# Kernel tuning notes

Measured on AMD Instinct MI355X. Metric: run time of the kernel, lower is better.

The kernel has to match this reference:

```python
import jax, jax.numpy as jnp
import numpy as np

HIDDEN = 2048
HEADS = 16
HEAD_DIM = HIDDEN // HEADS  # 128
ROPE_BASE = 10000.0
RMS_EPS = 1e-6
MINUS_INF = -10000.0


def rms_norm(x, w):
    xf = x.astype(jnp.float32)
    var = jnp.mean(xf * xf, axis=-1, keepdims=True)
    return w * (x * jax.lax.rsqrt(var + RMS_EPS))


def rotate_half(x):
    x1, x2 = jnp.split(x, 2, axis=-1)
    return jnp.concatenate((-x2, x1), axis=-1)


def rope_tables(seq_len, dtype):
    inv_freq = 1.0 / (ROPE_BASE ** (jnp.arange(0, HEAD_DIM, 2, dtype=jnp.float32) / HEAD_DIM))
    t = jnp.arange(seq_len, dtype=jnp.float32)
    freqs = jnp.einsum('i,j->ij', t, inv_freq)           # [S, D/2]
    emb = jnp.concatenate((freqs, freqs), axis=-1)       # [S, D]
    return jnp.cos(emb).astype(dtype), jnp.sin(emb).astype(dtype)


def setup_inputs() -> dict:
    key = jax.random.key(0)
    ks = jax.random.split(key, 6)
    B, S, H = 2, 2048, HIDDEN
    x = jax.random.normal(ks[0], (B, S, H), dtype=jnp.float32) * 0.5
    norm_w = jnp.ones((H,), dtype=jnp.float32)
    scale = 0.02
    wq = jax.random.normal(ks[1], (H, H), dtype=jnp.float32) * scale
    wk = jax.random.normal(ks[2], (H, H), dtype=jnp.float32) * scale
    wv = jax.random.normal(ks[3], (H, H), dtype=jnp.float32) * scale
    wo = jax.random.normal(ks[4], (H, H), dtype=jnp.float32) * scale
    position_ids = jnp.broadcast_to(jnp.arange(S, dtype=jnp.int32), (B, S))
    return {"x": x, "norm_w": norm_w, "wq": wq, "wk": wk, "wv": wv,
            "wo": wo, "position_ids": position_ids}


def reference(x, norm_w, wq, wk, wv, wo, position_ids):
    B, S, H = x.shape
    h = rms_norm(x, norm_w)
    # torch Linear: y = h @ W.T, weight is [out, in]
    def proj(w):
        return jnp.einsum('bsd,od->bso', h, w).reshape(B, S, HEADS, HEAD_DIM).transpose(0, 2, 1, 3)
    q, k, v = proj(wq), proj(wk), proj(wv)  # [B, Hh, S, D]
    cos, sin = rope_tables(S, x.dtype)
    cos = cos[position_ids][:, None]  # [B, 1, S, D]
    sin = sin[position_ids][:, None]
    q = q * cos + rotate_half(q) * sin
    k = k * cos + rotate_half(k) * sin
    scores = jnp.einsum('bhqd,bhkd->bhqk', q, k) / jnp.sqrt(jnp.float32(HEAD_DIM))
    causal = jnp.tril(jnp.ones((S, S), dtype=bool))
    scores = scores + jnp.where(causal, 0.0, MINUS_INF).astype(scores.dtype)
    probs = jax.nn.softmax(scores, axis=-1)
    ctx = jnp.einsum('bhqk,bhkd->bhqd', probs, v)          # [B, Hh, S, D]
    ctx = ctx.transpose(0, 2, 1, 3).reshape(B, S, H)
    out = jnp.einsum('bsd,od->bso', ctx, wo)
    return out
```

## Files before the change

kernel.cpp:

```cpp
#include <hip/hip_runtime.h>
#include <hip/hip_bf16.h>
#include <stdint.h>

#define S_LEN   2048
#define BATCH   2
#define HID     2048
#define NHEADS  16
#define HDIM    128
#define ROWS    (BATCH * S_LEN)
#define QS      6144
#define ATT_SCALE 0.08838834764831843f

typedef __attribute__((ext_vector_type(8))) short s16x8;
typedef __attribute__((ext_vector_type(4))) float f32x4;

#define GLL16(gp, lp)                                                          \
  __builtin_amdgcn_global_load_lds(                                            \
      (__attribute__((address_space(1))) void*)(gp),                           \
      (__attribute__((address_space(3))) void*)(lp), 16, 0, 0)

__device__ __forceinline__ float bf2f(unsigned short u) {
  union { unsigned int i; float f; } v; v.i = ((unsigned int)u) << 16; return v.f;
}
__device__ __forceinline__ unsigned short f2bf(float f) {
  union { float f; unsigned int i; } v; v.f = f;
  unsigned int i = v.i;
  return (unsigned short)((i + 0x7FFFu + ((i >> 16) & 1u)) >> 16);
}
__device__ __forceinline__ void store_out(unsigned short* p, float v) { *p = f2bf(v); }
__device__ __forceinline__ void store_out(float* p, float v) { *p = v; }

__global__ __launch_bounds__(256) void cast_w_kernel(const float* __restrict__ in,
                                                     unsigned short* __restrict__ out, int n4) {
  int i = blockIdx.x * 256 + threadIdx.x;
  if (i >= n4) return;
  float4 v = ((const float4*)in)[i];
  ushort4 o;
  o.x = f2bf(v.x); o.y = f2bf(v.y); o.z = f2bf(v.z); o.w = f2bf(v.w);
  ((ushort4*)out)[i] = o;
}

__global__ __launch_bounds__(256) void rmsnorm_kernel(const float* __restrict__ x,
                                                      const float* __restrict__ w,
                                                      unsigned short* __restrict__ h) {
  int row = blockIdx.x;
  int t = threadIdx.x;
  const float4* xr4 = (const float4*)(x + (size_t)row * HID);
  float4 a = xr4[t], b = xr4[t + 256];
  float ss = a.x*a.x + a.y*a.y + a.z*a.z + a.w*a.w
           + b.x*b.x + b.y*b.y + b.z*b.z + b.w*b.w;
#pragma unroll
  for (int off = 32; off >= 1; off >>= 1) ss += __shfl_xor(ss, off, 64);
  __shared__ float red[4];
  if ((t & 63) == 0) red[t >> 6] = ss;
  __syncthreads();
  float tot = red[0] + red[1] + red[2] + red[3];
  float rs = rsqrtf(tot * (1.0f / (float)HID) + 1e-6f);
  const float4* w4 = (const float4*)w;
  float4 wa = w4[t], wb = w4[t + 256];
  ushort4 oa, ob;
  oa.x = f2bf(a.x * wa.x * rs); oa.y = f2bf(a.y * wa.y * rs);
  oa.z = f2bf(a.z * wa.z * rs); oa.w = f2bf(a.w * wa.w * rs);
  ob.x = f2bf(b.x * wb.x * rs); ob.y = f2bf(b.y * wb.y * rs);
  ob.z = f2bf(b.z * wb.z * rs); ob.w = f2bf(b.w * wb.w * rs);
  ushort4* hr = (ushort4*)(h + (size_t)row * HID);
  hr[t] = oa; hr[t + 256] = ob;
}

__global__ void rope_tab_kernel(float* __restrict__ cost, float* __restrict__ sint) {
  int s = blockIdx.x, j = threadIdx.x;
  float inv = powf(10000.0f, -((float)j) / 64.0f);
  float ang = (float)s * inv;
  cost[s * 64 + j] = cosf(ang);
  sint[s * 64 + j] = sinf(ang);
}

__global__ __launch_bounds__(256) void rope_kernel(const int* __restrict__ pos_ids,
                                                   const float* __restrict__ cost,
                                                   const float* __restrict__ sint,
                                                   unsigned short* __restrict__ qkv) {
  int row = blockIdx.x;
  int p = pos_ids[row];
  int t = threadIdx.x;
  int head = t >> 4;
  int j0 = (t & 15) * 4;
  size_t base = (size_t)row * QS + head * HDIM;
  float4 c = *(const float4*)(cost + p * 64 + j0);
  float4 s = *(const float4*)(sint + p * 64 + j0);
#pragma unroll
  for (int which = 0; which < 2; which++) {
    unsigned short* ptr = qkv + base + which * HID;
    float sc = which ? 1.0f : ATT_SCALE;
    ushort4 v1 = *(ushort4*)(ptr + j0);
    ushort4 v2 = *(ushort4*)(ptr + 64 + j0);
    ushort4 o1, o2;
    o1.x = f2bf((bf2f(v1.x) * c.x - bf2f(v2.x) * s.x) * sc);
    o1.y = f2bf((bf2f(v1.y) * c.y - bf2f(v2.y) * s.y) * sc);
    o1.z = f2bf((bf2f(v1.z) * c.z - bf2f(v2.z) * s.z) * sc);
    o1.w = f2bf((bf2f(v1.w) * c.w - bf2f(v2.w) * s.w) * sc);
    o2.x = f2bf((bf2f(v2.x) * c.x + bf2f(v1.x) * s.x) * sc);
    o2.y = f2bf((bf2f(v2.y) * c.y + bf2f(v1.y) * s.y) * sc);
    o2.z = f2bf((bf2f(v2.z) * c.z + bf2f(v1.z) * s.z) * sc);
    o2.w = f2bf((bf2f(v2.w) * c.w + bf2f(v1.w) * s.w) * sc);
    *(ushort4*)(ptr + j0) = o1;
    *(ushort4*)(ptr + 64 + j0) = o2;
  }
}

__global__ __launch_bounds__(256) void transpose_v_kernel(const unsigned short* __restrict__ qkv,
                                                          unsigned short* __restrict__ vt) {
  __shared__ unsigned short tile[64][72];
  const int stile = blockIdx.x, dt = blockIdx.y, bh = blockIdx.z;
  const int t = threadIdx.x;
  const int b = bh >> 4, h = bh & 15;
  const int s0 = stile * 64;
  const unsigned short* src = qkv + (size_t)(b * S_LEN + s0) * QS + 2 * HID + h * HDIM + dt * 64;
#pragma unroll
  for (int it = 0; it < 2; it++) {
    int sl = (t >> 3) + 32 * it;
    int dl = (t & 7) * 8;
    *(s16x8*)&tile[sl][dl] = *(const s16x8*)(src + (size_t)sl * QS + dl);
  }
  __syncthreads();
#pragma unroll
  for (int it = 0; it < 2; it++) {
    int dl = (t >> 3) + 32 * it;
    int sl8 = (t & 7) * 8;
    s16x8 o;
#pragma unroll
    for (int jj = 0; jj < 8; jj++) o[jj] = (short)tile[sl8 + jj][dl];
    *(s16x8*)(vt + (size_t)(bh * 128 + dt * 64 + dl) * S_LEN + s0 + sl8) = o;
  }
}

#define SA(kt, bi) {                                                           \
    const unsigned short* s_ = aS + (size_t)(kt) * 64;                         \
    char* d_ = (char*)Ab[bi] + tid * 16;                                       \
    GLL16(s_, d_);                                                             \
    GLL16(s_ + (size_t)64 * K, d_ + 8192);                                     \
  }
#define SB(kt, bi, hf) {                                                       \
    const unsigned short* s_ = bS + (size_t)(hf) * 128 * K + (size_t)(kt) * 64;\
    char* d_ = (char*)Bb[bi] + (hf) * 16384 + tid * 16;                        \
    GLL16(s_, d_);                                                             \
    GLL16(s_ + (size_t)64 * K, d_ + 8192);                                     \
  }

template <typename OutT, int NI>
__global__ __launch_bounds__(512, 1) void gemm8_kernel(const unsigned short* __restrict__ A,
                                                       const unsigned short* __restrict__ B,
                                                       OutT* __restrict__ C, int K, int N) {
  __shared__ __align__(16) unsigned short Ab[3][128 * 64];
  __shared__ __align__(16) unsigned short Bb[3][NI * 64 * 64];
  const int bm = blockIdx.y, bn = blockIdx.x;
  const int tid = threadIdx.x;
  const int w = tid >> 6, wr = w >> 2, wc = w & 3;
  const int l = tid & 63, g = l >> 4, r = l & 15;
  const int KT = K >> 6;

  const int srow = tid >> 3;
  const int sgr = (tid & 7) ^ (srow & 7);
  const unsigned short* aS = A + (size_t)(bm * 128 + srow) * K + sgr * 8;
  const unsigned short* bS = B + (size_t)(bn * (NI * 64) + srow) * K + sgr * 8;

  f32x4 zero = {0.f, 0.f, 0.f, 0.f};
  f32x4 acc[4][NI];
#pragma unroll
  for (int mi = 0; mi < 4; mi++)
#pragma unroll
    for (int ni = 0; ni < NI; ni++) acc[mi][ni] = zero;

  const int swx = (r & 7) << 4;
  const int ks0 = (g << 4) ^ swx;
  const int ks1 = ((4 | g) << 4) ^ swx;
  const int aOff = (wr * 64 + r) * 128;
  const int bOff = (wc * (NI * 16) + r) * 128;

  SA(0, 0); SB(0, 0, 0); if (NI == 4) SB(0, 0, 1);
  SA(1, 1); SB(1, 1, 0); if (NI == 4) SB(1, 1, 1);

  int cur = 0;
  for (int kt = 0; kt < KT; ++kt) {
    const int b2 = (cur >= 1) ? cur - 1 : cur + 2;
    if (kt == KT - 1)      { asm volatile("s_waitcnt vmcnt(0)" ::: "memory"); }
    else if (NI == 4)      { asm volatile("s_waitcnt vmcnt(6)" ::: "memory"); }
    else                   { asm volatile("s_waitcnt vmcnt(4)" ::: "memory"); }
    __builtin_amdgcn_s_barrier();
    __builtin_amdgcn_sched_barrier(0);
    const char* lA = (const char*)Ab[cur];
    const char* lB = (const char*)Bb[cur];
    const bool more = (kt + 2 < KT);

    s16x8 a[4][2], b[NI][2];
#pragma unroll
    for (int mi = 0; mi < 4; mi++) {
      a[mi][0] = *(const s16x8*)(lA + aOff + mi * 2048 + ks0);
      a[mi][1] = *(const s16x8*)(lA + aOff + mi * 2048 + ks1);
    }
#pragma unroll
    for (int ni = 0; ni < NI / 2; ni++) {
      b[ni][0] = *(const s16x8*)(lB + bOff + ni * 2048 + ks0);
      b[ni][1] = *(const s16x8*)(lB + bOff + ni * 2048 + ks1);
    }
    if (more) { SA(kt + 2, b2); if (NI == 4) SB(kt + 2, b2, 0); }
    __builtin_amdgcn_s_setprio(1);
#pragma unroll
    for (int kk = 0; kk < 2; kk++)
#pragma unroll
      for (int ni = 0; ni < NI / 2; ni++)
#pragma unroll
        for (int mi = 0; mi < 4; mi++)
          acc[mi][ni] = __builtin_amdgcn_mfma_f32_16x16x32_bf16(a[mi][kk], b[ni][kk], acc[mi][ni], 0, 0, 0);
    __builtin_amdgcn_s_setprio(0);
    __builtin_amdgcn_sched_barrier(0);

#pragma unroll
    for (int ni = NI / 2; ni < NI; ni++) {
      b[ni][0] = *(const s16x8*)(lB + bOff + ni * 2048 + ks0);
      b[ni][1] = *(const s16x8*)(lB + bOff + ni * 2048 + ks1);
    }
    if (more) { if (NI == 4) { SB(kt + 2, b2, 1); } else { SB(kt + 2, b2, 0); } }
    __builtin_amdgcn_s_setprio(1);
#pragma unroll
    for (int kk = 0; kk < 2; kk++)
#pragma unroll
      for (int ni = NI / 2; ni < NI; ni++)
#pragma unroll
        for (int mi = 0; mi < 4; mi++)
          acc[mi][ni] = __builtin_amdgcn_mfma_f32_16x16x32_bf16(a[mi][kk], b[ni][kk], acc[mi][ni], 0, 0, 0);
    __builtin_amdgcn_s_setprio(0);
    cur = (cur == 2) ? 0 : cur + 1;
  }

#pragma unroll
  for (int mi = 0; mi < 4; mi++)
#pragma unroll
    for (int ni = 0; ni < NI; ni++) {
      const int crow = bm * 128 + wr * 64 + mi * 16 + g * 4;
      const int ccol = bn * (NI * 64) + wc * (NI * 16) + ni * 16 + r;
#pragma unroll
      for (int j = 0; j < 4; j++)
        store_out(&C[(size_t)(crow + j) * N + ccol], acc[mi][ni][j]);
    }
}

__global__ __launch_bounds__(256, 4) void attn_kernel(const unsigned short* __restrict__ QKV,
                                                      const unsigned short* __restrict__ VT,
                                                      unsigned short* __restrict__ O) {
  __shared__ __align__(16) unsigned short Ksm[64 * 128];
  __shared__ __align__(16) unsigned short VTsm[128 * 64];
  __shared__ __align__(16) unsigned short Psm[4 * 16 * 64];
  const int bid = blockIdx.x;
  const int grp = bid & 7, idx = bid >> 3;
  const int qt = 31 - (idx >> 2);
  const int bh = (grp << 2) | (idx & 3);
  const int b = bh >> 4, hd = bh & 15;
  const int tid = threadIdx.x, w = tid >> 6, l = tid & 63, g = l >> 4, r = l & 15;
  const int qbs = qt * 64 + w * 16;

  const unsigned short* qp = QKV + (size_t)(b * S_LEN + qbs + r) * QS + hd * HDIM;
  s16x8 qf[4];
#pragma unroll
  for (int ks = 0; ks < 4; ks++) qf[ks] = *(const s16x8*)(qp + ks * 32 + g * 8);

  float mreg[4], lreg[4];
  f32x4 zero = {0.f, 0.f, 0.f, 0.f};
  f32x4 oacc[8];
#pragma unroll
  for (int jj = 0; jj < 4; jj++) { mreg[jj] = -1e30f; lreg[jj] = 0.f; }
#pragma unroll
  for (int di = 0; di < 8; di++) oacc[di] = zero;

  const int cK = tid & 15, rowK = tid >> 4;
  const unsigned short* kp_base = QKV + (size_t)(b * S_LEN + rowK) * QS + HID + hd * HDIM
                                  + ((cK ^ (rowK & 7)) << 3);
  const int cV = tid & 7, dV = tid >> 3;
  const unsigned short* vp_base = VT + (size_t)(bh * 128 + dV) * S_LEN + ((cV ^ (dV & 7)) << 3);
  char* const ksm_c = (char*)Ksm;
  char* const vtsm_c = (char*)VTsm;
  char* const psm_w = (char*)Psm + w * 2048;

#define STAGE(kt)                                                              \
  {                                                                            \
    const unsigned short* kp_ = kp_base + (size_t)((kt) * 64) * QS;            \
    const unsigned short* vp_ = vp_base + (kt) * 64;                           \
    GLL16(kp_,                      ksm_c + tid * 16);                         \
    GLL16(kp_ + (size_t)16 * QS,    ksm_c + (tid + 256) * 16);                 \
    GLL16(kp_ + (size_t)32 * QS,    ksm_c + (tid + 512) * 16);                 \
    GLL16(kp_ + (size_t)48 * QS,    ksm_c + (tid + 768) * 16);                 \
    GLL16(vp_,                      vtsm_c + tid * 16);                        \
    GLL16(vp_ + (size_t)32 * S_LEN, vtsm_c + (tid + 256) * 16);                \
    GLL16(vp_ + (size_t)64 * S_LEN, vtsm_c + (tid + 512) * 16);                \
    GLL16(vp_ + (size_t)96 * S_LEN, vtsm_c + (tid + 768) * 16);                \
  }

  const int nt = qt + 1;
  STAGE(0);

  for (int kt2 = 0; kt2 < nt; kt2++) {
    asm volatile("s_waitcnt vmcnt(0)" ::: "memory");
    __builtin_amdgcn_s_barrier();
    __builtin_amdgcn_sched_barrier(0);

    f32x4 sacc[4];
#pragma unroll
    for (int ni = 0; ni < 4; ni++) sacc[ni] = zero;
#pragma unroll
    for (int ni = 0; ni < 4; ni++) {
      const int krow = ni * 16 + r;
      const int swz = (krow & 7) << 4;
      const char* kb2 = ksm_c + krow * 256;
#pragma unroll
      for (int ks = 0; ks < 4; ks++) {
        s16x8 kf = *(const s16x8*)(kb2 + ((ks * 64 + g * 16) ^ swz));
        sacc[ni] = __builtin_amdgcn_mfma_f32_16x16x32_bf16(qf[ks], kf, sacc[ni], 0, 0, 0);
      }
    }

    const bool domask = (kt2 == qt);
    float mrow[4];
#pragma unroll
    for (int jj = 0; jj < 4; jj++) mrow[jj] = -1e30f;
#pragma unroll
    for (int ni = 0; ni < 4; ni++)
#pragma unroll
      for (int jj = 0; jj < 4; jj++) {
        float sval = sacc[ni][jj];
        if (domask && (kt2 * 64 + ni * 16 + r) > (qbs + g * 4 + jj)) sval = -1e30f;
        sacc[ni][jj] = sval;
        mrow[jj] = fmaxf(mrow[jj], sval);
      }
#pragma unroll
    for (int jj = 0; jj < 4; jj++) {
#pragma unroll
      for (int off = 8; off >= 1; off >>= 1)
        mrow[jj] = fmaxf(mrow[jj], __shfl_xor(mrow[jj], off, 64));
    }
    float corr[4];
#pragma unroll
    for (int jj = 0; jj < 4; jj++) {
      float mn = fmaxf(mreg[jj], mrow[jj]);
      corr[jj] = __expf(mreg[jj] - mn);
      mreg[jj] = mn;
      float sm = 0.f;
#pragma unroll
      for (int ni = 0; ni < 4; ni++) {
        float p2 = __expf(sacc[ni][jj] - mn);
        sacc[ni][jj] = p2;
        sm += p2;
      }
#pragma unroll
      for (int off = 8; off >= 1; off >>= 1) sm += __shfl_xor(sm, off, 64);
      lreg[jj] = lreg[jj] * corr[jj] + sm;
    }
#pragma unroll
    for (int di = 0; di < 8; di++)
#pragma unroll
      for (int jj = 0; jj < 4; jj++) oacc[di][jj] *= corr[jj];

#pragma unroll
    for (int ni = 0; ni < 4; ni++)
#pragma unroll
      for (int jj = 0; jj < 4; jj++) {
        int prow = g * 4 + jj;
        int byte = (prow * 128 + ((ni * 16 + r) << 1)) ^ ((prow & 7) << 4);
        *(unsigned short*)(psm_w + byte) = f2bf(sacc[ni][jj]);
      }

#pragma unroll
    for (int ksl = 0; ksl < 2; ksl++) {
      s16x8 pa = *(const s16x8*)(psm_w + ((r * 128 + ((ksl * 32 + g * 8) << 1)) ^ ((r & 7) << 4)));
      const int kgran = ksl * 4 + g;
#pragma unroll
      for (int di = 0; di < 8; di++) {
        const int d = di * 16 + r;
        s16x8 vf = *(const s16x8*)(vtsm_c + d * 128 + ((kgran ^ (d & 7)) << 4));
        oacc[di] = __builtin_amdgcn_mfma_f32_16x16x32_bf16(pa, vf, oacc[di], 0, 0, 0);
      }
    }

    __builtin_amdgcn_s_barrier();
    if (kt2 + 1 < nt) STAGE(kt2 + 1);
  }
#undef STAGE

#pragma unroll
  for (int di = 0; di < 8; di++)
#pragma unroll
    for (int jj = 0; jj < 4; jj++) {
      int orow = qbs + g * 4 + jj;
      O[(size_t)(b * S_LEN + orow) * HID + hd * HDIM + di * 16 + r] =
          f2bf(oacc[di][jj] / lreg[jj]);
    }
}

extern "C" void kernel_launch(void* const* d_in, const int* in_sizes, int n_in,
                              void* d_out, int out_size, void* d_ws, size_t ws_size,
                              hipStream_t stream) {
  const float* x      = (const float*)d_in[0];
  const float* norm_w = (const float*)d_in[1];
  const float* wq     = (const float*)d_in[2];
  const float* wk     = (const float*)d_in[3];
  const float* wv     = (const float*)d_in[4];
  const float* wo     = (const float*)d_in[5];
  const int*   pos    = (const int*)d_in[6];
  float* out = (float*)d_out;

  char* ws = (char*)d_ws;
  const size_t WQKV_B = (size_t)3 * HID * HID * 2;
  const size_t VT_B   = (size_t)ROWS * HID * 2;
  const size_t H_B    = (size_t)ROWS * HID * 2;
  const size_t QKV_B  = (size_t)ROWS * QS * 2;

  unsigned short* wqkvb = (unsigned short*)(ws);
  unsigned short* vt    = (unsigned short*)(ws);
  unsigned short* wob   = (unsigned short*)(ws + VT_B);
  unsigned short* h     = (unsigned short*)(ws + WQKV_B);
  unsigned short* qkv   = (unsigned short*)(ws + WQKV_B + H_B);
  float* cost = (float*)(ws + WQKV_B + H_B + QKV_B);
  float* sint = cost + (size_t)S_LEN * 64;

  const int n4 = HID * HID / 4;
  cast_w_kernel<<<n4 / 256, 256, 0, stream>>>(wq, wqkvb, n4);
  cast_w_kernel<<<n4 / 256, 256, 0, stream>>>(wk, wqkvb + (size_t)HID * HID, n4);
  cast_w_kernel<<<n4 / 256, 256, 0, stream>>>(wv, wqkvb + (size_t)2 * HID * HID, n4);
  rope_tab_kernel<<<S_LEN, 64, 0, stream>>>(cost, sint);
  rmsnorm_kernel<<<ROWS, 256, 0, stream>>>(x, norm_w, h);

  dim3 qkvgrid(QS / 256, ROWS / 128);
  gemm8_kernel<unsigned short, 4><<<qkvgrid, 512, 0, stream>>>(h, wqkvb, qkv, HID, QS);

  cast_w_kernel<<<n4 / 256, 256, 0, stream>>>(wo, wob, n4);
  dim3 tgrid(S_LEN / 64, 2, BATCH * NHEADS);
  transpose_v_kernel<<<tgrid, 256, 0, stream>>>(qkv, vt);

  rope_kernel<<<ROWS, 256, 0, stream>>>(pos, cost, sint, qkv);

  attn_kernel<<<1024, 256, 0, stream>>>(qkv, vt, h );

  dim3 ogrid(HID / 128, ROWS / 128);
  gemm8_kernel<float, 2><<<ogrid, 512, 0, stream>>>(h, wob, out, HID, HID);
}
```

Measured before the change: 298.2 us.

## Split QKV GEMM into 256x256-tile QK kernel plus V GEMM; fuse weight casts

Measured after the change: 295.1 us. About the same (-1.0%).

```diff
diff --git a/kernel.cpp b/kernel.cpp
--- a/kernel.cpp
+++ b/kernel.cpp
@@ -30,14 +30,20 @@
 __device__ __forceinline__ void store_out(unsigned short* p, float v) { *p = f2bf(v); }
 __device__ __forceinline__ void store_out(float* p, float v) { *p = v; }
 
-__global__ __launch_bounds__(256) void cast_w_kernel(const float* __restrict__ in,
-                                                     unsigned short* __restrict__ out, int n4) {
+__global__ __launch_bounds__(256) void cast4_kernel(const float* __restrict__ w0,
+                                                    const float* __restrict__ w1,
+                                                    const float* __restrict__ w2,
+                                                    const float* __restrict__ w3,
+                                                    unsigned short* __restrict__ dqkv,
+                                                    unsigned short* __restrict__ dwo) {
+  const int which = blockIdx.y;
+  const float* src = (which == 0) ? w0 : (which == 1) ? w1 : (which == 2) ? w2 : w3;
+  unsigned short* dst = (which < 3) ? dqkv + (size_t)which * HID * HID : dwo;
   int i = blockIdx.x * 256 + threadIdx.x;
-  if (i >= n4) return;
-  float4 v = ((const float4*)in)[i];
+  float4 v = ((const float4*)src)[i];
   ushort4 o;
   o.x = f2bf(v.x); o.y = f2bf(v.y); o.z = f2bf(v.z); o.w = f2bf(v.w);
-  ((ushort4*)out)[i] = o;
+  ((ushort4*)dst)[i] = o;
 }
 
 __global__ __launch_bounds__(256) void rmsnorm_kernel(const float* __restrict__ x,
@@ -133,6 +139,121 @@
   }
 }
 
+#define SH(kt, bi, kk2) {                                                      \
+    const unsigned short* sa_ = aQ + (size_t)(kt) * 64 + (kk2) * 32;           \
+    const unsigned short* sb_ = bQ + (size_t)(kt) * 64 + (kk2) * 32;           \
+    char* da_ = qsm + ((bi) * 2 + (kk2)) * 32768 + tid * 16;                   \
+    GLL16(sa_, da_);                                                           \
+    GLL16(sa_ + (size_t)128 * K, da_ + 8192);                                  \
+    GLL16(sb_, da_ + 16384);                                                   \
+    GLL16(sb_ + (size_t)128 * K, da_ + 16384 + 8192);                          \
+  }
+
+__global__ __launch_bounds__(512, 2) void gemm_qk_kernel(const unsigned short* __restrict__ A,
+                                                         const unsigned short* __restrict__ B,
+                                                         unsigned short* __restrict__ C,
+                                                         int K, int N) {
+  __shared__ __align__(16) unsigned short Qsm[2][2][2][256 * 32];
+  const int bm = blockIdx.y, bn = blockIdx.x;
+  const int tid = threadIdx.x;
+  const int w = tid >> 6, wr = w >> 2, wc = w & 3;
+  const int l = tid & 63, g = l >> 4, r = l & 15;
+  const int KT = K >> 6;
+
+  const int srow = tid >> 2;
+  const int sg = (tid & 3) ^ ((tid >> 2) & 3) ^ ((tid >> 4) & 3);
+  const unsigned short* aQ = A + (size_t)(bm * 256 + srow) * K + sg * 8;
+  const unsigned short* bQ = B + (size_t)(bn * 256 + srow) * K + sg * 8;
+  char* const qsm = (char*)Qsm;
+
+  f32x4 zero = {0.f, 0.f, 0.f, 0.f};
+  f32x4 acc[8][4];
+#pragma unroll
+  for (int mi = 0; mi < 8; mi++)
+#pragma unroll
+    for (int ni = 0; ni < 4; ni++) acc[mi][ni] = zero;
+
+  const int ro = ((g ^ (r & 3) ^ ((r >> 2) & 3)) << 4);
+  const int aOff = (wr * 128 + r) * 64 + ro;
+  const int bOff = 16384 + (wc * 64 + r) * 64 + ro;
+
+  SH(0, 0, 0); SH(0, 0, 1);
+
+  for (int kt = 0; kt < KT; ++kt) {
+    const int buf = kt & 1;
+    const bool more = (kt + 1 < KT);
+    const char* l0 = qsm + (buf * 2 + 0) * 32768;
+    const char* l1 = qsm + (buf * 2 + 1) * 32768;
+
+    asm volatile("s_waitcnt vmcnt(4)" ::: "memory");
+    __builtin_amdgcn_s_barrier();
+    __builtin_amdgcn_sched_barrier(0);
+    s16x8 a[4], b[4];
+#pragma unroll
+    for (int ni = 0; ni < 4; ni++) b[ni] = *(const s16x8*)(l0 + bOff + ni * 1024);
+#pragma unroll
+    for (int i = 0; i < 4; i++) a[i] = *(const s16x8*)(l0 + aOff + i * 1024);
+    if (more) SH(kt + 1, buf ^ 1, 0);
+    __builtin_amdgcn_s_setprio(1);
+#pragma unroll
+    for (int ni = 0; ni < 4; ni++)
+#pragma unroll
+      for (int i = 0; i < 4; i++)
+        acc[i][ni] = __builtin_amdgcn_mfma_f32_16x16x32_bf16(a[i], b[ni], acc[i][ni], 0, 0, 0);
+    __builtin_amdgcn_s_setprio(0);
+
+    s16x8 a2[4];
+#pragma unroll
+    for (int i = 0; i < 4; i++) a2[i] = *(const s16x8*)(l0 + aOff + (4 + i) * 1024);
+    __builtin_amdgcn_s_setprio(1);
+#pragma unroll
+    for (int ni = 0; ni < 4; ni++)
+#pragma unroll
+      for (int i = 0; i < 4; i++)
+        acc[4 + i][ni] = __builtin_amdgcn_mfma_f32_16x16x32_bf16(a2[i], b[ni], acc[4 + i][ni], 0, 0, 0);
+    __builtin_amdgcn_s_setprio(0);
+
+    if (more) { asm volatile("s_waitcnt vmcnt(4)" ::: "memory"); }
+    else      { asm volatile("s_waitcnt vmcnt(0)" ::: "memory"); }
+    __builtin_amdgcn_s_barrier();
+    __builtin_amdgcn_sched_barrier(0);
+#pragma unroll
+    for (int ni = 0; ni < 4; ni++) b[ni] = *(const s16x8*)(l1 + bOff + ni * 1024);
+#pragma unroll
+    for (int i = 0; i < 4; i++) a[i] = *(const s16x8*)(l1 + aOff + i * 1024);
+    if (more) SH(kt + 1, buf ^ 1, 1);
+    __builtin_amdgcn_s_setprio(1);
+#pragma unroll
+    for (int ni = 0; ni < 4; ni++)
+#pragma unroll
+      for (int i = 0; i < 4; i++)
+        acc[i][ni] = __builtin_amdgcn_mfma_f32_16x16x32_bf16(a[i], b[ni], acc[i][ni], 0, 0, 0);
+    __builtin_amdgcn_s_setprio(0);
+
+#pragma unroll
+    for (int i = 0; i < 4; i++) a2[i] = *(const s16x8*)(l1 + aOff + (4 + i) * 1024);
+    __builtin_amdgcn_s_setprio(1);
+#pragma unroll
+    for (int ni = 0; ni < 4; ni++)
+#pragma unroll
+      for (int i = 0; i < 4; i++)
+        acc[4 + i][ni] = __builtin_amdgcn_mfma_f32_16x16x32_bf16(a2[i], b[ni], acc[4 + i][ni], 0, 0, 0);
+    __builtin_amdgcn_s_setprio(0);
+  }
+
+#pragma unroll
+  for (int mi = 0; mi < 8; mi++)
+#pragma unroll
+    for (int ni = 0; ni < 4; ni++) {
+      const int crow = bm * 256 + wr * 128 + mi * 16 + g * 4;
+      const int ccol = bn * 256 + wc * 64 + ni * 16 + r;
+#pragma unroll
+      for (int j = 0; j < 4; j++)
+        store_out(&C[(size_t)(crow + j) * N + ccol], acc[mi][ni][j]);
+    }
+}
+#undef SH
+
 #define SA(kt, bi) {                                                           \
     const unsigned short* s_ = aS + (size_t)(kt) * 64;                         \
     char* d_ = (char*)Ab[bi] + tid * 16;                                       \
@@ -408,29 +529,30 @@
 
   char* ws = (char*)d_ws;
   const size_t WQKV_B = (size_t)3 * HID * HID * 2;
-  const size_t VT_B   = (size_t)ROWS * HID * 2;
+  const size_t WO_B   = (size_t)HID * HID * 2;
   const size_t H_B    = (size_t)ROWS * HID * 2;
   const size_t QKV_B  = (size_t)ROWS * QS * 2;
 
   unsigned short* wqkvb = (unsigned short*)(ws);
   unsigned short* vt    = (unsigned short*)(ws);
-  unsigned short* wob   = (unsigned short*)(ws + VT_B);
-  unsigned short* h     = (unsigned short*)(ws + WQKV_B);
-  unsigned short* qkv   = (unsigned short*)(ws + WQKV_B + H_B);
-  float* cost = (float*)(ws + WQKV_B + H_B + QKV_B);
+  unsigned short* wob   = (unsigned short*)(ws + WQKV_B);
+  unsigned short* h     = (unsigned short*)(ws + WQKV_B + WO_B);
+  unsigned short* qkv   = (unsigned short*)(ws + WQKV_B + WO_B + H_B);
+  float* cost = (float*)(ws + WQKV_B + WO_B + H_B + QKV_B);
   float* sint = cost + (size_t)S_LEN * 64;
 
-  const int n4 = HID * HID / 4;
-  cast_w_kernel<<<n4 / 256, 256, 0, stream>>>(wq, wqkvb, n4);
-  cast_w_kernel<<<n4 / 256, 256, 0, stream>>>(wk, wqkvb + (size_t)HID * HID, n4);
-  cast_w_kernel<<<n4 / 256, 256, 0, stream>>>(wv, wqkvb + (size_t)2 * HID * HID, n4);
+  dim3 cgrid(HID * HID / 4 / 256, 4);
+  cast4_kernel<<<cgrid, 256, 0, stream>>>(wq, wk, wv, wo, wqkvb, wob);
   rope_tab_kernel<<<S_LEN, 64, 0, stream>>>(cost, sint);
   rmsnorm_kernel<<<ROWS, 256, 0, stream>>>(x, norm_w, h);
 
-  dim3 qkvgrid(QS / 256, ROWS / 128);
-  gemm8_kernel<unsigned short, 4><<<qkvgrid, 512, 0, stream>>>(h, wqkvb, qkv, HID, QS);
-
-  cast_w_kernel<<<n4 / 256, 256, 0, stream>>>(wo, wob, n4);
+  dim3 qkgrid(2 * HID / 256, ROWS / 256);
+  gemm_qk_kernel<<<qkgrid, 512, 0, stream>>>(h, wqkvb, qkv, HID, QS);
+
+  dim3 vgrid(HID / 256, ROWS / 128);
+  gemm8_kernel<unsigned short, 4><<<vgrid, 512, 0, stream>>>(
+      h, wqkvb + (size_t)2 * HID * HID, qkv + 2 * HID, HID, QS);
+
   dim3 tgrid(S_LEN / 64, 2, BATCH * NHEADS);
   transpose_v_kernel<<<tgrid, 256, 0, stream>>>(qkv, vt);
 
```
